# Performance work log

Measured on AMD Instinct MI355X. Metric: run time of the kernel, lower is better.

## Reference

```python
import jax, jax.numpy as jnp
import numpy as np
from jax import lax

NQ = 12   # num_qubits
NL = 6    # num_layers
NC = 64   # num_classes
BATCH = 512
TWO_PI = 6.283185307179586


def _bcast(v):
    # broadcast a per-batch scalar (B,) against state (B, 2,...,2)
    return v.reshape((-1,) + (1,) * NQ) if v.ndim == 1 else v


def _apply_rx(state, theta, wire):
    """Apply RX(theta) on `wire`. state: (B,)+(2,)*NQ complex64.
    RX(t) = [[cos(t/2), -i sin(t/2)], [-i sin(t/2), cos(t/2)]]."""
    c = _bcast(jnp.cos(theta / 2))
    s = _bcast(jnp.sin(theta / 2))
    ax = 1 + wire  # wire 0 is the most significant qubit (PennyLane ordering)
    s0 = lax.index_in_dim(state, 0, ax, keepdims=True)
    s1 = lax.index_in_dim(state, 1, ax, keepdims=True)
    n0 = c * s0 - 1j * s * s1
    n1 = -1j * s * s0 + c * s1
    return jnp.concatenate([n0, n1], axis=ax)


def _apply_cnot(state, ctrl, tgt):
    ac, at = 1 + ctrl, 1 + tgt
    s0 = lax.index_in_dim(state, 0, ac, keepdims=True)
    s1 = lax.index_in_dim(state, 1, ac, keepdims=True)
    s1 = jnp.flip(s1, axis=at)  # X on target where control = 1
    return jnp.concatenate([s0, s1], axis=ac)


def _circuit(x, qweights):
    """AngleEmbedding (RX) + BasicEntanglerLayers (RX + ring CNOTs) -> <Z_i>."""
    B = x.shape[0]
    state = jnp.zeros((B,) + (2,) * NQ, jnp.complex64)
    state = state.at[(slice(None),) + (0,) * NQ].set(1.0)  # |0...0>
    # AngleEmbedding: RX(x[:, w]) on wire w (per-sample angles)
    for w in range(NQ):
        state = _apply_rx(state, x[:, w], w)
    # BasicEntanglerLayers: per layer RX rotations then ring of CNOTs
    for l in range(NL):
        for w in range(NQ):
            state = _apply_rx(state, qweights[l, w], w)
        for w in range(NQ):
            state = _apply_cnot(state, w, (w + 1) % NQ)
    probs = jnp.real(state) ** 2 + jnp.imag(state) ** 2  # (B, 2,...,2) float32
    zs = []
    for w in range(NQ):
        other = tuple(a for a in range(1, NQ + 1) if a != 1 + w)
        marg = probs.sum(axis=other)  # (B, 2)
        zs.append(marg[:, 0] - marg[:, 1])  # <Z_w>
    return jnp.stack(zs, axis=1)  # (B, NQ)


def setup_inputs() -> dict:
    key = jax.random.key(0)
    k1, k2, k3 = jax.random.split(key, 3)
    x = jax.random.normal(k1, (BATCH, NQ), dtype=jnp.float32)
    qweights = jax.random.uniform(k2, (NL, NQ), dtype=jnp.float32) * TWO_PI
    W = jax.random.normal(k3, (NC, NQ), dtype=jnp.float32) * 0.1
    b = jnp.zeros((NC,), dtype=jnp.float32)
    return {"x": x, "qweights": qweights, "W": W, "b": b}


def reference(x, qweights, W, b):
    z = _circuit(x, qweights)          # (B, NQ) expectation values
    return z @ W.T + b                  # (B, NC) classifier logits
```

## Files before the change

kernel.cpp:

```cpp
#include <hip/hip_runtime.h>

#define NQB   12
#define NST   4096
#define NLAY  6
#define NCLS  64
#define TPB   512
#define NGATE 84
#define MAXG  112

struct KArgs {
    int mlo[MAXG];
    int src[MAXG];
    int bstart[9];
    int tot;
    int meas[NQB];
};

__device__ __forceinline__ void fast_sincos(float phi, float* s, float* c) {
    float rv = phi * 0.15915494309189535f;
    rv -= floorf(rv);
    *s = __builtin_amdgcn_sinf(rv);
    *c = __builtin_amdgcn_cosf(rv);
}

__global__ __launch_bounds__(TPB) void qnn_kernel(
    const float* __restrict__ x, const float* __restrict__ qw,
    const float* __restrict__ W, const float* __restrict__ bias,
    float* __restrict__ out, KArgs A)
{
    __shared__ float2 d[NST];
    __shared__ float  gl[2 * MAXG];
    __shared__ float  zpart[TPB / 64][NQB];
    __shared__ float  zfin[NQB];

    const int tid = threadIdx.x;
    const int b   = blockIdx.x;

    if (tid < A.tot) {
        int s = A.src[tid];
        float v = 0.0f;
        if (s >= NQB)      v = 0.5f * qw[s - NQB];
        else if (s >= 0)   v = 0.5f * x[b * NQB + s];
        gl[2 * tid]     = v;
        gl[2 * tid + 1] = __int_as_float(A.mlo[tid]);
    }
    __syncthreads();

    float B[8];
    #pragma unroll
    for (int i = 0; i < 8; ++i) {
        float acc = 0.f;
        const int e = A.bstart[i + 1];
        for (int j = A.bstart[i]; j < e; j += 2) {
            float4 g2 = *(const float4*)&gl[2 * j];
            int m0 = __float_as_int(g2.y);
            int m1 = __float_as_int(g2.w);
            acc += (__popc(tid & m0) & 1) ? -g2.x : g2.x;
            acc += (__popc(tid & m1) & 1) ? -g2.z : g2.z;
        }
        B[i] = acc;
    }
    #pragma unroll
    for (int s2 = 1; s2 < 8; s2 <<= 1) {
        #pragma unroll
        for (int i = 0; i < 8; ++i)
            if (!(i & s2)) {
                float u = B[i], v = B[i | s2];
                B[i] = u + v; B[i | s2] = u - v;
            }
    }

    float2 myd[8];
    #pragma unroll
    for (int r = 0; r < 8; ++r) {
        float sv, cv;
        fast_sincos(B[r], &sv, &cv);
        myd[r] = make_float2(cv, sv);
        d[tid + (r << 9)] = myd[r];
    }
    __syncthreads();

    float acc[NQB];
    #pragma unroll
    for (int w = 0; w < NQB; ++w) acc[w] = 0.f;
    #pragma unroll
    for (int r = 0; r < 8; ++r) {
        const int k = tid + (r << 9);
        const float2 m = myd[r];
        #pragma unroll
        for (int w = 0; w < NQB; ++w) {
            float2 p = d[k ^ A.meas[w]];
            acc[w] = fmaf(m.x, p.x, fmaf(m.y, p.y, acc[w]));
        }
    }

    const int lane = tid & 63, wid = tid >> 6;
    #pragma unroll
    for (int w = 0; w < NQB; ++w) {
        float v = acc[w];
        #pragma unroll
        for (int off = 32; off > 0; off >>= 1) v += __shfl_down(v, off);
        if (lane == 0) zpart[wid][w] = v;
    }
    __syncthreads();
    if (tid < NQB) {
        float v = 0.f;
        #pragma unroll
        for (int k = 0; k < TPB / 64; ++k) v += zpart[k][tid];
        zfin[tid] = v * (1.0f / NST);
    }
    __syncthreads();

    if (tid < NCLS) {
        float a = bias[tid];
        #pragma unroll
        for (int w = 0; w < NQB; ++w) a += zfin[w] * W[tid * NQB + w];
        out[b * NCLS + tid] = a;
    }
}


static int f_of(int j) {
    for (int w = 11; w >= 0; --w) {
        int pc = 11 - w;
        int pt = 11 - ((w + 1) % 12);
        j ^= ((j >> pc) & 1) << pt;
    }
    return j;
}

static void build_args(KArgs* A) {
    int fm[NGATE], src[NGATE];
    for (int w = 0; w < NQB; ++w) { fm[w] = 1 << (11 - w); src[w] = w; }
    for (int l = 0; l < NLAY; ++l)
        for (int w = 0; w < NQB; ++w) {
            int v = 1 << (11 - w);
            for (int t = 0; t < l; ++t) v = f_of(v);
            fm[NQB + l * NQB + w]  = v;
            src[NQB + l * NQB + w] = NQB + l * NQB + w;
        }
    int tot = 0;
    for (int bkt = 0; bkt < 8; ++bkt) {
        A->bstart[bkt] = tot;
        for (int g = 0; g < NGATE; ++g)
            if ((fm[g] >> 9) == bkt) {
                A->mlo[tot] = fm[g] & 511;
                A->src[tot] = src[g];
                ++tot;
            }
        if (tot & 1) { A->mlo[tot] = 0; A->src[tot] = -1; ++tot; }
    }
    A->bstart[8] = tot;
    A->tot = tot;
    for (int g = tot; g < MAXG; ++g) { A->mlo[g] = 0; A->src[g] = -1; }

    int col[NQB];
    for (int k = 0; k < NQB; ++k) {
        int v = 1 << k;
        for (int t = 0; t < NLAY; ++t) v = f_of(v);
        col[k] = v;
    }
    unsigned rowG[NQB], rowH[NQB];
    for (int r = 0; r < NQB; ++r) {
        unsigned rr = 0;
        for (int k = 0; k < NQB; ++k) rr |= ((unsigned)((col[k] >> r) & 1)) << k;
        rowG[r] = rr;
        rowH[r] = 1u << r;
    }
    for (int k = 0; k < NQB; ++k) {
        int piv = -1;
        for (int r = k; r < NQB; ++r)
            if ((rowG[r] >> k) & 1) { piv = r; break; }
        unsigned tg = rowG[piv], th = rowH[piv];
        rowG[piv] = rowG[k]; rowH[piv] = rowH[k];
        rowG[k] = tg; rowH[k] = th;
        for (int r = 0; r < NQB; ++r)
            if (r != k && ((rowG[r] >> k) & 1)) { rowG[r] ^= rowG[k]; rowH[r] ^= rowH[k]; }
    }
    for (int w = 0; w < NQB; ++w) A->meas[w] = (int)rowH[11 - w];
}

extern "C" void kernel_launch(void* const* d_in, const int* in_sizes, int n_in,
                              void* d_out, int out_size, void* d_ws, size_t ws_size,
                              hipStream_t stream) {
    const float* x    = (const float*)d_in[0];
    const float* qw   = (const float*)d_in[1];
    const float* W    = (const float*)d_in[2];
    const float* bias = (const float*)d_in[3];
    float* out        = (float*)d_out;

    KArgs A;
    build_args(&A);

    const int batch = in_sizes[0] / NQB;
    qnn_kernel<<<batch, TPB, 0, stream>>>(x, qw, W, bias, out, A);
}
```

Measured before the change: 76.11 us.

## Precompute batch-independent weight phase table in separate kernel, reorder measurement loop

Moves the weight-dependent phase sum (72 parity terms per basis state) into a small pre-kernel that writes a 4096-entry table to workspace. The main kernel reads that table and adds only the per-sample embedding phase, computed separably from the thread index bits instead of through gate buckets and a Walsh butterfly. It also swaps the loop order of the measurement correlation so the XOR index is hoisted per wire. This adds a second launch and a global-memory round trip in exchange for removing per-block redundant work.

Result: faster. 72.54 us (-4.7%).

```diff
diff --git a/kernel.cpp b/kernel.cpp
--- a/kernel.cpp
+++ b/kernel.cpp
@@ -4,77 +4,62 @@
 #define NST   4096
 #define NLAY  6
 #define NCLS  64
+#define NGQ   72
 #define TPB   512
-#define NGATE 84
-#define MAXG  112
 
-struct KArgs {
-    int mlo[MAXG];
-    int src[MAXG];
-    int bstart[9];
-    int tot;
-    int meas[NQB];
-};
+struct PhiArgs  { int m[NGQ]; };
+struct MainArgs { int meas[NQB]; };
 
-__device__ __forceinline__ void fast_sincos(float phi, float* s, float* c) {
-    float rv = phi * 0.15915494309189535f;
-    rv -= floorf(rv);
-    *s = __builtin_amdgcn_sinf(rv);
-    *c = __builtin_amdgcn_cosf(rv);
+__global__ __launch_bounds__(64) void phiq_kernel(
+    const float* __restrict__ qw, float* __restrict__ phiq, PhiArgs A)
+{
+    const int k = blockIdx.x * 64 + threadIdx.x;
+    float acc = 0.f;
+    #pragma unroll
+    for (int g = 0; g < NGQ; ++g) {
+        float v = 0.5f * qw[g];
+        acc += (__popc(k & A.m[g]) & 1) ? -v : v;
+    }
+    phiq[k] = acc;
 }
 
 __global__ __launch_bounds__(TPB) void qnn_kernel(
-    const float* __restrict__ x, const float* __restrict__ qw,
+    const float* __restrict__ x, const float* __restrict__ phiq,
     const float* __restrict__ W, const float* __restrict__ bias,
-    float* __restrict__ out, KArgs A)
+    float* __restrict__ out, MainArgs A)
 {
     __shared__ float2 d[NST];
-    __shared__ float  gl[2 * MAXG];
     __shared__ float  zpart[TPB / 64][NQB];
     __shared__ float  zfin[NQB];
 
     const int tid = threadIdx.x;
     const int b   = blockIdx.x;
 
-    if (tid < A.tot) {
-        int s = A.src[tid];
-        float v = 0.0f;
-        if (s >= NQB)      v = 0.5f * qw[s - NQB];
-        else if (s >= 0)   v = 0.5f * x[b * NQB + s];
-        gl[2 * tid]     = v;
-        gl[2 * tid + 1] = __int_as_float(A.mlo[tid]);
-    }
-    __syncthreads();
+    float pq[8];
+    #pragma unroll
+    for (int r = 0; r < 8; ++r) pq[r] = phiq[tid + (r << 9)];
 
-    float B[8];
+    float xv[NQB];
     #pragma unroll
-    for (int i = 0; i < 8; ++i) {
-        float acc = 0.f;
-        const int e = A.bstart[i + 1];
-        for (int j = A.bstart[i]; j < e; j += 2) {
-            float4 g2 = *(const float4*)&gl[2 * j];
-            int m0 = __float_as_int(g2.y);
-            int m1 = __float_as_int(g2.w);
-            acc += (__popc(tid & m0) & 1) ? -g2.x : g2.x;
-            acc += (__popc(tid & m1) & 1) ? -g2.z : g2.z;
-        }
-        B[i] = acc;
-    }
+    for (int w = 0; w < NQB; ++w) xv[w] = 0.5f * x[b * NQB + w];
+    float base = 0.f;
     #pragma unroll
-    for (int s2 = 1; s2 < 8; s2 <<= 1) {
-        #pragma unroll
-        for (int i = 0; i < 8; ++i)
-            if (!(i & s2)) {
-                float u = B[i], v = B[i | s2];
-                B[i] = u + v; B[i | s2] = u - v;
-            }
-    }
+    for (int w = 3; w < NQB; ++w)
+        base += ((tid >> (11 - w)) & 1) ? -xv[w] : xv[w];
+    float c3[8];
+    #pragma unroll
+    for (int r = 0; r < 8; ++r)
+        c3[r] = ((r & 4) ? -xv[0] : xv[0]) + ((r & 2) ? -xv[1] : xv[1])
+              + ((r & 1) ? -xv[2] : xv[2]);
 
     float2 myd[8];
     #pragma unroll
     for (int r = 0; r < 8; ++r) {
-        float sv, cv;
-        fast_sincos(B[r], &sv, &cv);
+        float phi = pq[r] + base + c3[r];
+        float rv = phi * 0.15915494309189535f;
+        rv -= floorf(rv);
+        float sv = __builtin_amdgcn_sinf(rv);
+        float cv = __builtin_amdgcn_cosf(rv);
         myd[r] = make_float2(cv, sv);
         d[tid + (r << 9)] = myd[r];
     }
@@ -84,13 +69,12 @@
     #pragma unroll
     for (int w = 0; w < NQB; ++w) acc[w] = 0.f;
     #pragma unroll
-    for (int r = 0; r < 8; ++r) {
-        const int k = tid + (r << 9);
-        const float2 m = myd[r];
+    for (int w = 0; w < NQB; ++w) {
+        const int u = tid ^ A.meas[w];
         #pragma unroll
-        for (int w = 0; w < NQB; ++w) {
-            float2 p = d[k ^ A.meas[w]];
-            acc[w] = fmaf(m.x, p.x, fmaf(m.y, p.y, acc[w]));
+        for (int r = 0; r < 8; ++r) {
+            float2 p = d[u ^ (r << 9)];
+            acc[w] = fmaf(myd[r].x, p.x, fmaf(myd[r].y, p.y, acc[w]));
         }
     }
 
@@ -129,31 +113,13 @@
     return j;
 }
 
-static void build_args(KArgs* A) {
-    int fm[NGATE], src[NGATE];
-    for (int w = 0; w < NQB; ++w) { fm[w] = 1 << (11 - w); src[w] = w; }
+static void build_args(PhiArgs* P, MainArgs* M) {
     for (int l = 0; l < NLAY; ++l)
         for (int w = 0; w < NQB; ++w) {
             int v = 1 << (11 - w);
             for (int t = 0; t < l; ++t) v = f_of(v);
-            fm[NQB + l * NQB + w]  = v;
-            src[NQB + l * NQB + w] = NQB + l * NQB + w;
+            P->m[l * NQB + w] = v;
         }
-    int tot = 0;
-    for (int bkt = 0; bkt < 8; ++bkt) {
-        A->bstart[bkt] = tot;
-        for (int g = 0; g < NGATE; ++g)
-            if ((fm[g] >> 9) == bkt) {
-                A->mlo[tot] = fm[g] & 511;
-                A->src[tot] = src[g];
-                ++tot;
-            }
-        if (tot & 1) { A->mlo[tot] = 0; A->src[tot] = -1; ++tot; }
-    }
-    A->bstart[8] = tot;
-    A->tot = tot;
-    for (int g = tot; g < MAXG; ++g) { A->mlo[g] = 0; A->src[g] = -1; }
-
     int col[NQB];
     for (int k = 0; k < NQB; ++k) {
         int v = 1 << k;
@@ -177,7 +143,7 @@
         for (int r = 0; r < NQB; ++r)
             if (r != k && ((rowG[r] >> k) & 1)) { rowG[r] ^= rowG[k]; rowH[r] ^= rowH[k]; }
     }
-    for (int w = 0; w < NQB; ++w) A->meas[w] = (int)rowH[11 - w];
+    for (int w = 0; w < NQB; ++w) M->meas[w] = (int)rowH[11 - w];
 }
 
 extern "C" void kernel_launch(void* const* d_in, const int* in_sizes, int n_in,
@@ -188,10 +154,12 @@
     const float* W    = (const float*)d_in[2];
     const float* bias = (const float*)d_in[3];
     float* out        = (float*)d_out;
+    float* phiq       = (float*)d_ws;
 
-    KArgs A;
-    build_args(&A);
+    PhiArgs P; MainArgs M;
+    build_args(&P, &M);
 
     const int batch = in_sizes[0] / NQB;
-    qnn_kernel<<<batch, TPB, 0, stream>>>(x, qw, W, bias, out, A);
+    phiq_kernel<<<64, 64, 0, stream>>>(qw, phiq, P);
+    qnn_kernel<<<batch, TPB, 0, stream>>>(x, phiq, W, bias, out, M);
 }
```
